# Performance work log

Measured on AMD Instinct MI355X. Metric: run time of the kernel, lower is better.

Reference implementation:

```python
import jax, jax.numpy as jnp
import numpy as np
import math

B, S, D = 8, 2048, 512
H, DH = 8, 64  # heads, head dim

def setup_inputs() -> dict:
    key = jax.random.key(0)
    ks = jax.random.split(key, 13)
    w = 0.02
    return {
        "x_Q": jax.random.normal(ks[0], (B, S, D), jnp.float32),
        "x_K": jax.random.normal(ks[1], (B, S, D), jnp.float32),
        "x_V": jax.random.normal(ks[2], (B, S, D), jnp.float32),
        "Wq": jax.random.normal(ks[3], (H * DH, D), jnp.float32) * w,
        "bq": jnp.zeros((H * DH,), jnp.float32),
        "Wk": jax.random.normal(ks[4], (H * DH, D), jnp.float32) * w,
        "bk": jnp.zeros((H * DH,), jnp.float32),
        "Wv": jax.random.normal(ks[5], (H * DH, D), jnp.float32) * w,
        "bv": jnp.zeros((H * DH,), jnp.float32),
        "Wo": jax.random.normal(ks[6], (D, H * DH), jnp.float32) * w,
        "bo": jnp.zeros((D,), jnp.float32),
        "src_batch_lens": jax.random.randint(ks[7], (B,), 1, S + 1, jnp.int32),
    }

def reference(x_Q, x_K, x_V, Wq, bq, Wk, bk, Wv, bv, Wo, bo, src_batch_lens):
    b, s, _ = x_Q.shape
    # projections (torch Linear: x @ W.T + b), split into heads
    Q = (x_Q @ Wq.T + bq).reshape(b, s, H, DH)
    K = (x_K @ Wk.T + bk).reshape(b, s, H, DH)
    V = (x_V @ Wv.T + bv).reshape(b, s, H, DH)
    scale = 1.0 / math.sqrt(DH)
    # [b, h, q, k] scores
    scores = jnp.einsum('bqhd,bkhd->bhqk', Q * scale, K)
    # padding mask on key positions >= src_batch_lens[i], filled with -1e9
    key_mask = jnp.arange(s)[None, :] >= src_batch_lens[:, None]  # [b, k]
    scores = jnp.where(key_mask[:, None, None, :], -1.0e9, scores)
    attn = jax.nn.softmax(scores, axis=-1)  # dropout p=0.0 -> identity
    ctx = jnp.einsum('bhqk,bkhd->bqhd', attn, V).reshape(b, s, H * DH)
    return ctx @ Wo.T + bo
```

## Files before the change

kernel.cpp:

```cpp
#include <hip/hip_runtime.h>
#include <math.h>

#define NB 8
#define NS 2048
#define ND 512
#define NHH 8
#define NDH 64

typedef __attribute__((ext_vector_type(4))) float f32x4;
typedef __attribute__((ext_vector_type(8))) short bf16x8;
typedef unsigned short ush;

__device__ inline ush f2bf_rne(float f) {
    unsigned u = __float_as_uint(f);
    unsigned r = u + 0x7FFFu + ((u >> 16) & 1u);
    return (ush)(r >> 16);
}
__device__ inline float bf2f(ush h) { return __uint_as_float(((unsigned)h) << 16); }

__device__ inline unsigned cvt_pk_bf16(float lo, float hi) {
    unsigned r;
    asm("v_cvt_pk_bf16_f32 %0, %1, %2" : "=v"(r) : "v"(lo), "v"(hi));
    return r;
}

#if defined(__has_builtin)
#if __has_builtin(__builtin_amdgcn_exp2f)
#define EXP2F(x) __builtin_amdgcn_exp2f(x)
#else
#define EXP2F(x) exp2f(x)
#endif
#else
#define EXP2F(x) exp2f(x)
#endif

#define GLL16(gp, lp) __builtin_amdgcn_global_load_lds( \
    (const __attribute__((address_space(1))) unsigned int*)(gp), \
    (__attribute__((address_space(3))) unsigned int*)(lp), 16, 0, 0)

__global__ __launch_bounds__(256) void conv_w_kernel(
    const float* __restrict__ Wq, const float* __restrict__ Wk,
    const float* __restrict__ Wv, const float* __restrict__ Wo,
    ush* __restrict__ wbf, ush* __restrict__ wo_hi, ush* __restrict__ wo_lo)
{
    const int y = blockIdx.y;
    const int i = (blockIdx.x * 256 + threadIdx.x) * 4;
    if (y < 3) {
        const float* src = (y == 0) ? Wq : (y == 1) ? Wk : Wv;
        const float4 v = *(const float4*)&src[i];
        ushort4 o;
        o.x = f2bf_rne(v.x); o.y = f2bf_rne(v.y);
        o.z = f2bf_rne(v.z); o.w = f2bf_rne(v.w);
        *(ushort4*)&wbf[y * 262144 + i] = o;
    } else {
        const float4 v = *(const float4*)&Wo[i];
        ushort4 hi, lo;
        hi.x = f2bf_rne(v.x); lo.x = f2bf_rne(v.x - bf2f(hi.x));
        hi.y = f2bf_rne(v.y); lo.y = f2bf_rne(v.y - bf2f(hi.y));
        hi.z = f2bf_rne(v.z); lo.z = f2bf_rne(v.z - bf2f(hi.z));
        hi.w = f2bf_rne(v.w); lo.w = f2bf_rne(v.w - bf2f(hi.w));
        *(ushort4*)&wo_hi[i] = hi;
        *(ushort4*)&wo_lo[i] = lo;
    }
}

__global__ __launch_bounds__(256) void qkv_gemm_kernel(
    const float* __restrict__ xq, const float* __restrict__ xk, const float* __restrict__ xv,
    const ush* __restrict__ wbf,
    const float* __restrict__ bq, const float* __restrict__ bk, const float* __restrict__ bv,
    ush* __restrict__ Qb, ush* __restrict__ Kb, ush* __restrict__ VT)
{
    __shared__ ush As[2][4096];
    __shared__ ush Bs[2][4096];

    const int z = blockIdx.z;
    const float* X    = (z == 0) ? xq : (z == 1) ? xk : xv;
    const ush*   W    = wbf + z * 262144;
    const float* bias = (z == 0) ? bq : (z == 1) ? bk : bv;

    const int t = threadIdx.x;
    const int w = t >> 6, l = t & 63;
    const int l15 = l & 15, g = l >> 4;
    const int m0 = blockIdx.y * 128, n0 = blockIdx.x * 128;
    const int wm = (w & 1) << 6, wn = (w >> 1) << 6;

    const int srow = l >> 2;
    const int sg   = (l & 3) ^ ((srow + (srow >> 2)) & 3);
    const int fsw  = (g ^ ((l15 + (l15 >> 2)) & 3)) << 3;
    const int c0   = w * 2;

    f32x4 acc[4][4];
    #pragma unroll
    for (int i = 0; i < 4; ++i)
        #pragma unroll
        for (int j = 0; j < 4; ++j) acc[i][j] = (f32x4)(0.0f);

    auto packA = [&](const float4& a0, const float4& a1, const float4& a2,
                     const float4& a3, uint4& u0, uint4& u1) {
        u0.x = cvt_pk_bf16(a0.x, a0.y);
        u0.y = cvt_pk_bf16(a0.z, a0.w);
        u0.z = cvt_pk_bf16(a1.x, a1.y);
        u0.w = cvt_pk_bf16(a1.z, a1.w);
        u1.x = cvt_pk_bf16(a2.x, a2.y);
        u1.y = cvt_pk_bf16(a2.z, a2.w);
        u1.z = cvt_pk_bf16(a3.x, a3.y);
        u1.w = cvt_pk_bf16(a3.z, a3.w);
    };

    {
        const size_t ar0 = (size_t)(m0 + c0 * 16 + srow) * 512 + sg * 8;
        const size_t ar1 = (size_t)(m0 + (c0 + 1) * 16 + srow) * 512 + sg * 8;
        const float4 a0 = *(const float4*)&X[ar0];
        const float4 a1 = *(const float4*)&X[ar0 + 4];
        const float4 a2 = *(const float4*)&X[ar1];
        const float4 a3 = *(const float4*)&X[ar1 + 4];
        GLL16(&W[(size_t)(n0 + c0 * 16 + srow) * 512 + sg * 8], &Bs[0][c0 * 512 + l * 8]);
        GLL16(&W[(size_t)(n0 + (c0 + 1) * 16 + srow) * 512 + sg * 8], &Bs[0][(c0 + 1) * 512 + l * 8]);
        uint4 u0, u1;
        packA(a0, a1, a2, a3, u0, u1);
        *(uint4*)&As[0][c0 * 512 + l * 8] = u0;
        *(uint4*)&As[0][(c0 + 1) * 512 + l * 8] = u1;
        __syncthreads();
    }

    for (int ki = 0; ki < 16; ++ki) {
        const int buf = ki & 1;
        const int ktn = (ki + 1) * 32;
        float4 a0, a1, a2, a3;
        if (ki < 15) {
            const size_t ar0 = (size_t)(m0 + c0 * 16 + srow) * 512 + ktn + sg * 8;
            const size_t ar1 = (size_t)(m0 + (c0 + 1) * 16 + srow) * 512 + ktn + sg * 8;
            a0 = *(const float4*)&X[ar0];
            a1 = *(const float4*)&X[ar0 + 4];
            a2 = *(const float4*)&X[ar1];
            a3 = *(const float4*)&X[ar1 + 4];
            GLL16(&W[(size_t)(n0 + c0 * 16 + srow) * 512 + ktn + sg * 8], &Bs[buf ^ 1][c0 * 512 + l * 8]);
            GLL16(&W[(size_t)(n0 + (c0 + 1) * 16 + srow) * 512 + ktn + sg * 8], &Bs[buf ^ 1][(c0 + 1) * 512 + l * 8]);
        }

        bf16x8 af[4], bfr[4];
        #pragma unroll
        for (int mi = 0; mi < 4; ++mi)
            af[mi] = *(const bf16x8*)&As[buf][(((w & 1) << 2) + mi) * 512 + l15 * 32 + fsw];
        #pragma unroll
        for (int ni = 0; ni < 4; ++ni)
            bfr[ni] = *(const bf16x8*)&Bs[buf][(((w >> 1) << 2) + ni) * 512 + l15 * 32 + fsw];
        #pragma unroll
        for (int mi = 0; mi < 4; ++mi)
            #pragma unroll
            for (int ni = 0; ni < 4; ++ni)
                acc[mi][ni] = __builtin_amdgcn_mfma_f32_16x16x32_bf16(af[mi], bfr[ni], acc[mi][ni], 0, 0, 0);

        if (ki < 15) {
            uint4 u0, u1;
            packA(a0, a1, a2, a3, u0, u1);
            *(uint4*)&As[buf ^ 1][c0 * 512 + l * 8] = u0;
            *(uint4*)&As[buf ^ 1][(c0 + 1) * 512 + l * 8] = u1;
        }
        __syncthreads();
    }

    const float qscale = (z == 0) ? 0.18033688011112042f : 1.0f;
    float bnv[4];
    #pragma unroll
    for (int ni = 0; ni < 4; ++ni) bnv[ni] = bias[n0 + wn + ni * 16 + l15];

    if (z < 2) {
        ush* O = (z == 0) ? Qb : Kb;
        #pragma unroll
        for (int mi = 0; mi < 4; ++mi) {
            #pragma unroll
            for (int ni = 0; ni < 4; ++ni) {
                const int n = n0 + wn + ni * 16 + l15;
                const int hh = n >> 6, dh = n & 63;
                const int mb = m0 + wm + mi * 16 + (g << 2);
                const int bi = mb >> 11, s = mb & (NS - 1);
                const size_t base = ((size_t)(bi * 8 + hh) * 2048 + s) * 64 + dh;
                const unsigned u01 = cvt_pk_bf16((acc[mi][ni][0] + bnv[ni]) * qscale,
                                                 (acc[mi][ni][1] + bnv[ni]) * qscale);
                const unsigned u23 = cvt_pk_bf16((acc[mi][ni][2] + bnv[ni]) * qscale,
                                                 (acc[mi][ni][3] + bnv[ni]) * qscale);
                O[base]           = (ush)u01;
                O[base + 64]      = (ush)(u01 >> 16);
                O[base + 128]     = (ush)u23;
                O[base + 192]     = (ush)(u23 >> 16);
            }
        }
    } else {
        #pragma unroll
        for (int mi = 0; mi < 4; ++mi) {
            #pragma unroll
            for (int ni = 0; ni < 4; ++ni) {
                const int n = n0 + wn + ni * 16 + l15;
                const int hh = n >> 6, dh = n & 63;
                const int mb = m0 + wm + mi * 16 + (g << 2);
                const int bi = mb >> 11, s = mb & (NS - 1);
                uint2 pk;
                pk.x = cvt_pk_bf16(acc[mi][ni][0] + bnv[ni], acc[mi][ni][1] + bnv[ni]);
                pk.y = cvt_pk_bf16(acc[mi][ni][2] + bnv[ni], acc[mi][ni][3] + bnv[ni]);
                *(uint2*)&VT[((size_t)(bi * 8 + hh) * 64 + dh) * 2048 + s] = pk;
            }
        }
    }
}

__global__ __launch_bounds__(256) void attn_kernel(
    ush* __restrict__ Qb, const ush* __restrict__ Kb,
    const ush* __restrict__ VT, const int* __restrict__ lens,
    ush* __restrict__ ctx_lo)
{
    __shared__ ush Ps[128 * 72];
    __shared__ ush Vt[2 * 4624];

    const int tid = threadIdx.x;
    const int w = tid >> 6, l = tid & 63;
    const int l15 = l & 15, g = l >> 4;

    const int id = blockIdx.x;

    int Ls[8];
    #pragma unroll
    for (int j = 0; j < 8; ++j) Ls[j] = lens[j];
    const int slot = id >> 7;
    int b = 0;
    #pragma unroll
    for (int bb = 0; bb < 8; ++bb) {
        int r = 0;
        #pragma unroll
        for (int j = 0; j < 8; ++j)
            r += (Ls[j] > Ls[bb]) || (Ls[j] == Ls[bb] && j < bb);
        if (r == slot) b = bb;
    }
    const int h = id & 7, qt = (id >> 3) & 15;
    const int L = Ls[b];
    const int q0 = qt << 7;
    const size_t bh = ((size_t)b * 8 + h) * 2048;

    const ush* qptr = Qb + (bh + q0 + w * 16 + l15) * 64 + g * 8;
    const bf16x8 qfa0 = *(const bf16x8*)(qptr);
    const bf16x8 qfa1 = *(const bf16x8*)(qptr + 32);
    const bf16x8 qfb0 = *(const bf16x8*)(qptr + 64 * 64);
    const bf16x8 qfb1 = *(const bf16x8*)(qptr + 64 * 64 + 32);

    const ush* kbase = Kb + (bh + l15) * 64 + g * 8;

    const int dv = tid >> 2, seg = (tid & 3) << 4;
    const ush* vbase = VT + bh * 64 + (size_t)dv * 2048 + seg;
    const int vt_off = dv * 72 + ((dv >> 4) << 3) + seg;

    ush* psw_a = &Ps[(w * 16 + l15) * 72 + (g << 2)];
    const ush* pp_a = &Ps[(w * 16 + l15) * 72 + g * 8];
    ush* psw_b = psw_a + 64 * 72;
    const ush* pp_b = pp_a + 64 * 72;

    bf16x8 ones;
    #pragma unroll
    for (int j = 0; j < 8; ++j) ones[j] = (short)0x3F80;

    f32x4 oa[4], ob[4];
    f32x4 ola = (f32x4)(0.0f), olb = (f32x4)(0.0f);
    #pragma unroll
    for (int i = 0; i < 4; ++i) { oa[i] = (f32x4)(0.0f); ob[i] = (f32x4)(0.0f); }

    f32x4 spa[4], spb[4];
    const int T = (L + 63) >> 6;

    {
        const uint4 v0 = *(const uint4*)(vbase);
        const uint4 v1 = *(const uint4*)(vbase + 8);
        #pragma unroll
        for (int st = 0; st < 4; ++st) { spa[st] = (f32x4)(0.0f); spb[st] = (f32x4)(0.0f); }
        __builtin_amdgcn_s_setprio(1);
        #pragma unroll
        for (int st = 0; st < 4; ++st) {
            const bf16x8 kf0 = *(const bf16x8*)(kbase + st * 1024);
            const bf16x8 kf1 = *(const bf16x8*)(kbase + st * 1024 + 32);
            spa[st] = __builtin_amdgcn_mfma_f32_16x16x32_bf16(kf0, qfa0, spa[st], 0, 0, 0);
            spa[st] = __builtin_amdgcn_mfma_f32_16x16x32_bf16(kf1, qfa1, spa[st], 0, 0, 0);
            spb[st] = __builtin_amdgcn_mfma_f32_16x16x32_bf16(kf0, qfb0, spb[st], 0, 0, 0);
            spb[st] = __builtin_amdgcn_mfma_f32_16x16x32_bf16(kf1, qfb1, spb[st], 0, 0, 0);
        }
        __builtin_amdgcn_s_setprio(0);
        ush* dst = &Vt[vt_off];
        *(uint4*)dst = v0;
        *(uint4*)(dst + 8) = v1;
        __syncthreads();
    }

    auto finish = [&](const ush* vb, bool masked, int kb0) {
        uint2 pka[4], pkb[4];
        #pragma unroll
        for (int st = 0; st < 4; ++st) {
            float pa[4], pb[4];
            #pragma unroll
            for (int r = 0; r < 4; ++r) {
                float ea = EXP2F(spa[st][r]);
                float eb = EXP2F(spb[st][r]);
                if (masked) {
                    const int key = kb0 + st * 16 + (g << 2) + r;
                    ea = (key < L) ? ea : 0.0f;
                    eb = (key < L) ? eb : 0.0f;
                }
                pa[r] = ea; pb[r] = eb;
            }
            pka[st].x = cvt_pk_bf16(pa[0], pa[1]);
            pka[st].y = cvt_pk_bf16(pa[2], pa[3]);
            pkb[st].x = cvt_pk_bf16(pb[0], pb[1]);
            pkb[st].y = cvt_pk_bf16(pb[2], pb[3]);
        }
        #pragma unroll
        for (int st = 0; st < 4; ++st) {
            *(uint2*)(psw_a + st * 16) = pka[st];
            *(uint2*)(psw_b + st * 16) = pkb[st];
        }
        const bf16x8 pfa0 = *(const bf16x8*)(pp_a);
        const bf16x8 pfa1 = *(const bf16x8*)(pp_a + 32);
        const bf16x8 pfb0 = *(const bf16x8*)(pp_b);
        const bf16x8 pfb1 = *(const bf16x8*)(pp_b + 32);
        __builtin_amdgcn_s_setprio(1);
        ola = __builtin_amdgcn_mfma_f32_16x16x32_bf16(pfa0, ones, ola, 0, 0, 0);
        ola = __builtin_amdgcn_mfma_f32_16x16x32_bf16(pfa1, ones, ola, 0, 0, 0);
        olb = __builtin_amdgcn_mfma_f32_16x16x32_bf16(pfb0, ones, olb, 0, 0, 0);
        olb = __builtin_amdgcn_mfma_f32_16x16x32_bf16(pfb1, ones, olb, 0, 0, 0);
        #pragma unroll
        for (int st2 = 0; st2 < 4; ++st2) {
            const ush* vp = vb + (st2 * 16 + l15) * 72 + (st2 << 3) + g * 8;
            const bf16x8 vf0 = *(const bf16x8*)(vp);
            const bf16x8 vf1 = *(const bf16x8*)(vp + 32);
            oa[st2] = __builtin_amdgcn_mfma_f32_16x16x32_bf16(pfa0, vf0, oa[st2], 0, 0, 0);
            oa[st2] = __builtin_amdgcn_mfma_f32_16x16x32_bf16(pfa1, vf1, oa[st2], 0, 0, 0);
            ob[st2] = __builtin_amdgcn_mfma_f32_16x16x32_bf16(pfb0, vf0, ob[st2], 0, 0, 0);
            ob[st2] = __builtin_amdgcn_mfma_f32_16x16x32_bf16(pfb1, vf1, ob[st2], 0, 0, 0);
        }
        __builtin_amdgcn_s_setprio(0);
    };

    for (int t = 1; t < T; ++t) {
        const int k0 = t << 6;
        bf16x8 kf[8];
        const ush* kp = kbase + (size_t)k0 * 64;
        #pragma unroll
        for (int st = 0; st < 4; ++st) {
            kf[2 * st]     = *(const bf16x8*)(kp + st * 1024);
            kf[2 * st + 1] = *(const bf16x8*)(kp + st * 1024 + 32);
        }
        const uint4 nv0 = *(const uint4*)(vbase + k0);
        const uint4 nv1 = *(const uint4*)(vbase + k0 + 8);

        finish(&Vt[((t & 1) ^ 1) * 4624], false, 0);

        #pragma unroll
        for (int st = 0; st < 4; ++st) { spa[st] = (f32x4)(0.0f); spb[st] = (f32x4)(0.0f); }
        __builtin_amdgcn_s_setprio(1);
        #pragma unroll
        for (int st = 0; st < 4; ++st) {
            spa[st] = __builtin_amdgcn_mfma_f32_16x16x32_bf16(kf[2 * st], qfa0, spa[st], 0, 0, 0);
            spa[st] = __builtin_amdgcn_mfma_f32_16x16x32_bf16(kf[2 * st + 1], qfa1, spa[st], 0, 0, 0);
            spb[st] = __builtin_amdgcn_mfma_f32_16x16x32_bf16(kf[2 * st], qfb0, spb[st], 0, 0, 0);
            spb[st] = __builtin_amdgcn_mfma_f32_16x16x32_bf16(kf[2 * st + 1], qfb1, spb[st], 0, 0, 0);
        }
        __builtin_amdgcn_s_setprio(0);

        ush* dst = &Vt[(t & 1) * 4624 + vt_off];
        *(uint4*)dst = nv0;
        *(uint4*)(dst + 8) = nv1;
        __syncthreads();
    }

    finish(&Vt[((T - 1) & 1) * 4624], true, (T - 1) << 6);

    #pragma unroll
    for (int r = 0; r < 4; ++r) {
        const float inva = 1.0f / ola[r];
        const float invb = 1.0f / olb[r];
        const size_t rowa = bh + q0 + w * 16 + (g << 2) + r;
        const size_t rowb = rowa + 64;
        #pragma unroll
        for (int st2 = 0; st2 < 4; ++st2) {
            const float va = oa[st2][r] * inva;
            const ush ha = f2bf_rne(va);
            Qb[rowa * 64 + st2 * 16 + l15] = ha;
            ctx_lo[rowa * 64 + st2 * 16 + l15] = f2bf_rne(va - bf2f(ha));
            const float vbv = ob[st2][r] * invb;
            const ush hb = f2bf_rne(vbv);
            Qb[rowb * 64 + st2 * 16 + l15] = hb;
            ctx_lo[rowb * 64 + st2 * 16 + l15] = f2bf_rne(vbv - bf2f(hb));
        }
    }
}

__global__ __launch_bounds__(512) void out_gemm_kernel(
    const ush* __restrict__ ctx_hi, const ush* __restrict__ ctx_lo,
    const ush* __restrict__ wo_hi, const ush* __restrict__ wo_lo,
    const float* __restrict__ bo, float* __restrict__ out)
{
    __shared__ ush Ah[2][4096], Al[2][4096], Bh[2][4096], Bl[2][4096];

    const int t = threadIdx.x;
    const int w = t >> 6, l = t & 63;
    const int l15 = l & 15, g = l >> 4;
    const int m0 = blockIdx.y * 128, n0 = blockIdx.x * 128;
    const int wm = (w & 1) << 6, wn = (w >> 1) << 5;

    const int srow = l >> 2;
    const int sg   = (l & 3) ^ ((srow + (srow >> 2)) & 3);
    const int fsw  = (g ^ ((l15 + (l15 >> 2)) & 3)) << 3;
    const int c0   = w;

    f32x4 acc[4][2];
    #pragma unroll
    for (int i = 0; i < 4; ++i)
        #pragma unroll
        for (int j = 0; j < 2; ++j) acc[i][j] = (f32x4)(0.0f);

    auto stage = [&](int bf, int kt) {
        const int c = c0;
        const int m = m0 + c * 16 + srow;
        const int k = kt + sg * 8;
        const size_t ga = ((size_t)((m >> 11) * 8 + (k >> 6)) * 2048 + (m & (NS - 1))) * 64 + (k & 63);
        GLL16(&ctx_hi[ga], &Ah[bf][c * 512 + l * 8]);
        GLL16(&ctx_lo[ga], &Al[bf][c * 512 + l * 8]);
        const size_t gb = (size_t)(n0 + c * 16 + srow) * 512 + kt + sg * 8;
        GLL16(&wo_hi[gb], &Bh[bf][c * 512 + l * 8]);
        GLL16(&wo_lo[gb], &Bl[bf][c * 512 + l * 8]);
    };

    stage(0, 0);
    __syncthreads();

    for (int ki = 0; ki < 16; ++ki) {
        const int buf = ki & 1;
        if (ki < 15) stage(buf ^ 1, (ki + 1) * 32);

        bf16x8 ah[4], al[4], bh4[2], bl4[2];
        #pragma unroll
        for (int mi = 0; mi < 4; ++mi) {
            const int off = (((w & 1) << 2) + mi) * 512 + l15 * 32 + fsw;
            ah[mi] = *(const bf16x8*)&Ah[buf][off];
            al[mi] = *(const bf16x8*)&Al[buf][off];
        }
        #pragma unroll
        for (int ni = 0; ni < 2; ++ni) {
            const int off = (((w >> 1) << 1) + ni) * 512 + l15 * 32 + fsw;
            bh4[ni] = *(const bf16x8*)&Bh[buf][off];
            bl4[ni] = *(const bf16x8*)&Bl[buf][off];
        }
        #pragma unroll
        for (int mi = 0; mi < 4; ++mi)
            #pragma unroll
            for (int ni = 0; ni < 2; ++ni) {
                acc[mi][ni] = __builtin_amdgcn_mfma_f32_16x16x32_bf16(ah[mi], bh4[ni], acc[mi][ni], 0, 0, 0);
                acc[mi][ni] = __builtin_amdgcn_mfma_f32_16x16x32_bf16(al[mi], bh4[ni], acc[mi][ni], 0, 0, 0);
                acc[mi][ni] = __builtin_amdgcn_mfma_f32_16x16x32_bf16(ah[mi], bl4[ni], acc[mi][ni], 0, 0, 0);
            }
        __syncthreads();
    }

    float bov[2];
    #pragma unroll
    for (int ni = 0; ni < 2; ++ni) bov[ni] = bo[n0 + wn + ni * 16 + l15];

    #pragma unroll
    for (int mi = 0; mi < 4; ++mi)
        #pragma unroll
        for (int ni = 0; ni < 2; ++ni) {
            const int n = n0 + wn + ni * 16 + l15;
            #pragma unroll
            for (int r = 0; r < 4; ++r) {
                const int m = m0 + wm + mi * 16 + (g << 2) + r;
                out[(size_t)m * 512 + n] = acc[mi][ni][r] + bov[ni];
            }
        }
}

extern "C" void kernel_launch(void* const* d_in, const int* in_sizes, int n_in,
                              void* d_out, int out_size, void* d_ws, size_t ws_size,
                              hipStream_t stream)
{
    const float* xq   = (const float*)d_in[0];
    const float* xk   = (const float*)d_in[1];
    const float* xv   = (const float*)d_in[2];
    const float* Wq   = (const float*)d_in[3];
    const float* bq   = (const float*)d_in[4];
    const float* Wk   = (const float*)d_in[5];
    const float* bk   = (const float*)d_in[6];
    const float* Wv   = (const float*)d_in[7];
    const float* bv   = (const float*)d_in[8];
    const float* Wo   = (const float*)d_in[9];
    const float* bo   = (const float*)d_in[10];
    const int*   lens = (const int*)d_in[11];
    float* out = (float*)d_out;

    const size_t elems = (size_t)NB * NHH * NS * NDH;
    ush* Qb     = (ush*)d_ws;
    ush* Kb     = Qb + elems;
    ush* VT     = Kb + elems;
    ush* ctx_lo = VT + elems;
    ush* wbf    = ctx_lo + elems;
    ush* wo_hi  = wbf + 3 * 262144;
    ush* wo_lo  = wo_hi + 262144;

    const dim3 blk(256);
    conv_w_kernel<<<dim3(256, 4), blk, 0, stream>>>(Wq, Wk, Wv, Wo, wbf, wo_hi, wo_lo);
    qkv_gemm_kernel<<<dim3(4, 128, 3), blk, 0, stream>>>(
        xq, xk, xv, wbf, bq, bk, bv, Qb, Kb, VT);
    attn_kernel<<<dim3(NB * NHH * (NS / 128)), blk, 0, stream>>>(Qb, Kb, VT, lens, ctx_lo);
    out_gemm_kernel<<<dim3(4, 128), dim3(512), 0, stream>>>(Qb, ctx_lo, wo_hi, wo_lo, bo, out);
}
```

Before: 302.0 us.

## Pre-convert activations to bf16 and swizzle GEMM block order for L2 reuse

Adds a separate kernel that converts x_Q/x_K/x_V to bf16 in scratch buffers (reusing the output buffer and ctx_lo as temporary space). The QKV GEMM can then load A tiles with direct global-to-LDS loads instead of register loads plus in-loop conversion. Both GEMMs also remap the 1D block index so groups of 8 M-tiles share each N-tile, aiming for better L2 locality. The trade-off is an extra launch and an extra fp32 read plus bf16 write of the inputs.

```diff
diff --git a/kernel.cpp b/kernel.cpp
--- a/kernel.cpp
+++ b/kernel.cpp
@@ -64,8 +64,24 @@
     }
 }
 
+__global__ __launch_bounds__(256) void conv_x_kernel(
+    const float* __restrict__ xq, const float* __restrict__ xk,
+    const float* __restrict__ xv,
+    ush* __restrict__ xqb, ush* __restrict__ xkb, ush* __restrict__ xvb)
+{
+    const int y = blockIdx.y;
+    const float* src = (y == 0) ? xq : (y == 1) ? xk : xv;
+    ush* dst = (y == 0) ? xqb : (y == 1) ? xkb : xvb;
+    const size_t i = ((size_t)blockIdx.x * 256 + threadIdx.x) * 4;
+    const float4 v = *(const float4*)&src[i];
+    uint2 p;
+    p.x = cvt_pk_bf16(v.x, v.y);
+    p.y = cvt_pk_bf16(v.z, v.w);
+    *(uint2*)&dst[i] = p;
+}
+
 __global__ __launch_bounds__(256) void qkv_gemm_kernel(
-    const float* __restrict__ xq, const float* __restrict__ xk, const float* __restrict__ xv,
+    const ush* __restrict__ xqb, const ush* __restrict__ xkb, const ush* __restrict__ xvb,
     const ush* __restrict__ wbf,
     const float* __restrict__ bq, const float* __restrict__ bk, const float* __restrict__ bv,
     ush* __restrict__ Qb, ush* __restrict__ Kb, ush* __restrict__ VT)
@@ -74,14 +90,17 @@
     __shared__ ush Bs[2][4096];
 
     const int z = blockIdx.z;
-    const float* X    = (z == 0) ? xq : (z == 1) ? xk : xv;
+    const ush*   XA   = (z == 0) ? xqb : (z == 1) ? xkb : xvb;
     const ush*   W    = wbf + z * 262144;
     const float* bias = (z == 0) ? bq : (z == 1) ? bk : bv;
 
     const int t = threadIdx.x;
     const int w = t >> 6, l = t & 63;
     const int l15 = l & 15, g = l >> 4;
-    const int m0 = blockIdx.y * 128, n0 = blockIdx.x * 128;
+
+    const int j = blockIdx.x;
+    const int m0 = ((j & 7) + (j >> 5) * 8) * 128;
+    const int n0 = ((j >> 3) & 3) * 128;
     const int wm = (w & 1) << 6, wn = (w >> 1) << 6;
 
     const int srow = l >> 2;
@@ -93,50 +112,21 @@
     #pragma unroll
     for (int i = 0; i < 4; ++i)
         #pragma unroll
-        for (int j = 0; j < 4; ++j) acc[i][j] = (f32x4)(0.0f);
-
-    auto packA = [&](const float4& a0, const float4& a1, const float4& a2,
-                     const float4& a3, uint4& u0, uint4& u1) {
-        u0.x = cvt_pk_bf16(a0.x, a0.y);
-        u0.y = cvt_pk_bf16(a0.z, a0.w);
-        u0.z = cvt_pk_bf16(a1.x, a1.y);
-        u0.w = cvt_pk_bf16(a1.z, a1.w);
-        u1.x = cvt_pk_bf16(a2.x, a2.y);
-        u1.y = cvt_pk_bf16(a2.z, a2.w);
-        u1.z = cvt_pk_bf16(a3.x, a3.y);
-        u1.w = cvt_pk_bf16(a3.z, a3.w);
+        for (int jj = 0; jj < 4; ++jj) acc[i][jj] = (f32x4)(0.0f);
+
+    auto stage = [&](int bf, int kt) {
+        GLL16(&XA[(size_t)(m0 + c0 * 16 + srow) * 512 + kt + sg * 8], &As[bf][c0 * 512 + l * 8]);
+        GLL16(&XA[(size_t)(m0 + (c0 + 1) * 16 + srow) * 512 + kt + sg * 8], &As[bf][(c0 + 1) * 512 + l * 8]);
+        GLL16(&W[(size_t)(n0 + c0 * 16 + srow) * 512 + kt + sg * 8], &Bs[bf][c0 * 512 + l * 8]);
+        GLL16(&W[(size_t)(n0 + (c0 + 1) * 16 + srow) * 512 + kt + sg * 8], &Bs[bf][(c0 + 1) * 512 + l * 8]);
     };
 
-    {
-        const size_t ar0 = (size_t)(m0 + c0 * 16 + srow) * 512 + sg * 8;
-        const size_t ar1 = (size_t)(m0 + (c0 + 1) * 16 + srow) * 512 + sg * 8;
-        const float4 a0 = *(const float4*)&X[ar0];
-        const float4 a1 = *(const float4*)&X[ar0 + 4];
-        const float4 a2 = *(const float4*)&X[ar1];
-        const float4 a3 = *(const float4*)&X[ar1 + 4];
-        GLL16(&W[(size_t)(n0 + c0 * 16 + srow) * 512 + sg * 8], &Bs[0][c0 * 512 + l * 8]);
-        GLL16(&W[(size_t)(n0 + (c0 + 1) * 16 + srow) * 512 + sg * 8], &Bs[0][(c0 + 1) * 512 + l * 8]);
-        uint4 u0, u1;
-        packA(a0, a1, a2, a3, u0, u1);
-        *(uint4*)&As[0][c0 * 512 + l * 8] = u0;
-        *(uint4*)&As[0][(c0 + 1) * 512 + l * 8] = u1;
-        __syncthreads();
-    }
+    stage(0, 0);
+    __syncthreads();
 
     for (int ki = 0; ki < 16; ++ki) {
         const int buf = ki & 1;
-        const int ktn = (ki + 1) * 32;
-        float4 a0, a1, a2, a3;
-        if (ki < 15) {
-            const size_t ar0 = (size_t)(m0 + c0 * 16 + srow) * 512 + ktn + sg * 8;
-            const size_t ar1 = (size_t)(m0 + (c0 + 1) * 16 + srow) * 512 + ktn + sg * 8;
-            a0 = *(const float4*)&X[ar0];
-            a1 = *(const float4*)&X[ar0 + 4];
-            a2 = *(const float4*)&X[ar1];
-            a3 = *(const float4*)&X[ar1 + 4];
-            GLL16(&W[(size_t)(n0 + c0 * 16 + srow) * 512 + ktn + sg * 8], &Bs[buf ^ 1][c0 * 512 + l * 8]);
-            GLL16(&W[(size_t)(n0 + (c0 + 1) * 16 + srow) * 512 + ktn + sg * 8], &Bs[buf ^ 1][(c0 + 1) * 512 + l * 8]);
-        }
+        if (ki < 15) stage(buf ^ 1, (ki + 1) * 32);
 
         bf16x8 af[4], bfr[4];
         #pragma unroll
@@ -151,12 +141,6 @@
             for (int ni = 0; ni < 4; ++ni)
                 acc[mi][ni] = __builtin_amdgcn_mfma_f32_16x16x32_bf16(af[mi], bfr[ni], acc[mi][ni], 0, 0, 0);
 
-        if (ki < 15) {
-            uint4 u0, u1;
-            packA(a0, a1, a2, a3, u0, u1);
-            *(uint4*)&As[buf ^ 1][c0 * 512 + l * 8] = u0;
-            *(uint4*)&As[buf ^ 1][(c0 + 1) * 512 + l * 8] = u1;
-        }
         __syncthreads();
     }
 
@@ -399,7 +383,10 @@
     const int t = threadIdx.x;
     const int w = t >> 6, l = t & 63;
     const int l15 = l & 15, g = l >> 4;
-    const int m0 = blockIdx.y * 128, n0 = blockIdx.x * 128;
+
+    const int j = blockIdx.x;
+    const int m0 = ((j & 7) + (j >> 5) * 8) * 128;
+    const int n0 = ((j >> 3) & 3) * 128;
     const int wm = (w & 1) << 6, wn = (w >> 1) << 5;
 
     const int srow = l >> 2;
@@ -411,7 +398,7 @@
     #pragma unroll
     for (int i = 0; i < 4; ++i)
         #pragma unroll
-        for (int j = 0; j < 2; ++j) acc[i][j] = (f32x4)(0.0f);
+        for (int jj = 0; jj < 2; ++jj) acc[i][jj] = (f32x4)(0.0f);
 
     auto stage = [&](int bf, int kt) {
         const int c = c0;
@@ -500,10 +487,15 @@
     ush* wo_hi  = wbf + 3 * 262144;
     ush* wo_lo  = wo_hi + 262144;
 
+    ush* xqb = (ush*)out;
+    ush* xkb = xqb + elems;
+    ush* xvb = ctx_lo;
+
     const dim3 blk(256);
     conv_w_kernel<<<dim3(256, 4), blk, 0, stream>>>(Wq, Wk, Wv, Wo, wbf, wo_hi, wo_lo);
-    qkv_gemm_kernel<<<dim3(4, 128, 3), blk, 0, stream>>>(
-        xq, xk, xv, wbf, bq, bk, bv, Qb, Kb, VT);
+    conv_x_kernel<<<dim3(8192, 3), blk, 0, stream>>>(xq, xk, xv, xqb, xkb, xvb);
+    qkv_gemm_kernel<<<dim3(512, 1, 3), blk, 0, stream>>>(
+        xqb, xkb, xvb, wbf, bq, bk, bv, Qb, Kb, VT);
     attn_kernel<<<dim3(NB * NHH * (NS / 128)), blk, 0, stream>>>(Qb, Kb, VT, lens, ctx_lo);
-    out_gemm_kernel<<<dim3(4, 128), dim3(512), 0, stream>>>(Qb, ctx_lo, wo_hi, wo_lo, bo, out);
-}
+    out_gemm_kernel<<<dim3(512), dim3(512), 0, stream>>>(Qb, ctx_lo, wo_hi, wo_lo, bo, out);
+}
```

Result: no change. 299.5 us (-0.8%).
